# Kernel tuning notes

Hardware: AMD Instinct MI355X
Metric: run time of the kernel (lower is better)

The kernel has to match this reference:

```python
import jax, jax.numpy as jnp
from jax import lax
import numpy as np

DN = ('NCDHW', 'OIDHW', 'NCDHW')


def _conv3(x, w, b):
    # standard 3x3x3 conv, stride 1, pad 1
    y = lax.conv_general_dilated(x, w, (1, 1, 1), ((1, 1), (1, 1), (1, 1)), dimension_numbers=DN)
    return y + b[None, :, None, None, None]


def _bn(x, gamma, beta, eps=1e-5):
    # training-mode batchnorm over (N, D, H, W), biased variance (torch semantics)
    mean = jnp.mean(x, axis=(0, 2, 3, 4), keepdims=True)
    var = jnp.var(x, axis=(0, 2, 3, 4), keepdims=True)
    return gamma[None, :, None, None, None] * (x - mean) * lax.rsqrt(var + eps) + beta[None, :, None, None, None]


def _deform_conv(x, off, w):
    # ConvOffset3d: one scalar offset per deformable group shifting the temporal (D)
    # sampling position of every kernel tap; linear interpolation along D, zero padding.
    N, C, D, H, W = x.shape
    G = off.shape[1]
    cpg = C // G
    offc = jnp.repeat(off, cpg, axis=1)                        # [N,C,D,H,W]
    base = offc + jnp.arange(D, dtype=x.dtype)[None, None, :, None, None]
    out = None
    for kd in range(3):                                        # 3 temporal taps
        pos = base + (kd - 1)                                  # fractional sample pos along D
        f0 = jnp.floor(pos)
        frac = pos - f0
        i0 = f0.astype(jnp.int32)
        i1 = i0 + 1
        m0 = ((i0 >= 0) & (i0 < D)).astype(x.dtype)
        m1 = ((i1 >= 0) & (i1 < D)).astype(x.dtype)
        g = (jnp.take_along_axis(x, jnp.clip(i0, 0, D - 1), axis=2) * ((1.0 - frac) * m0)
             + jnp.take_along_axis(x, jnp.clip(i1, 0, D - 1), axis=2) * (frac * m1))
        # the D-shift for tap kd is already baked into g -> conv with kernel (1,3,3)
        y = lax.conv_general_dilated(g, w[:, :, kd:kd + 1], (1, 1, 1), ((0, 0), (1, 1), (1, 1)), dimension_numbers=DN)
        out = y if out is None else out + y
    return out


def setup_inputs() -> dict:
    key = jax.random.key(0)
    ks = jax.random.split(key, 4)
    C, cpg = 64, 8
    N, D, H, W = 8, 16, 56, 56
    G = C // cpg
    s = 1.0 / np.sqrt(C * 27).astype(np.float32)
    x = jax.random.normal(ks[0], (N, C, D, H, W), jnp.float32)
    w_off = jax.random.normal(ks[1], (G, C, 3, 3, 3), jnp.float32) * s
    b_off = jnp.zeros((G,), jnp.float32)
    w1 = jax.random.normal(ks[2], (C, C, 3, 3, 3), jnp.float32) * s
    w2 = jax.random.normal(ks[3], (C, C, 3, 3, 3), jnp.float32) * s
    b2 = jnp.zeros((C,), jnp.float32)
    return dict(x=x, w_off=w_off, b_off=b_off, w1=w1, w2=w2, b2=b2,
                bn1_gamma=jnp.ones((C,), jnp.float32), bn1_beta=jnp.zeros((C,), jnp.float32),
                bn2_gamma=jnp.ones((C,), jnp.float32), bn2_beta=jnp.zeros((C,), jnp.float32))


def reference(x, w_off, b_off, w1, w2, b2, bn1_gamma, bn1_beta, bn2_gamma, bn2_beta):
    off = _conv3(x, w_off, b_off)               # [N, G, D, H, W]
    out = _deform_conv(x, off, w1)              # deformable conv (no bias)
    out = jax.nn.relu(_bn(out, bn1_gamma, bn1_beta))
    out = _conv3(out, w2, b2)
    out = _bn(out, bn2_gamma, bn2_beta) + x     # residual
    out = jax.nn.relu(out)
    return (out, off)
```

## Files before the change

kernel.cpp:

```cpp
#include <hip/hip_runtime.h>

#define HW 3136
#define DHW 50176
#define NEL 25690112
#define CNT 401408.0f

typedef __attribute__((ext_vector_type(8))) short          short8;
typedef __attribute__((ext_vector_type(8))) unsigned short ushort8;
typedef __attribute__((ext_vector_type(4))) float          f32x4;

__device__ __forceinline__ unsigned f2bf(float f) {
    union { float f; unsigned u; } v; v.f = f;
    return (v.u + 0x7FFFu + ((v.u >> 16) & 1u)) >> 16;
}
__device__ __forceinline__ float bf2f(unsigned u) {
    union { unsigned u; float f; } v; v.u = u << 16;
    return v.f;
}
__device__ __forceinline__ unsigned cvt_pk_bf16(float lo, float hi) {
    unsigned r;
    asm("v_cvt_pk_bf16_f32 %0, %1, %2" : "=v"(r) : "v"(lo), "v"(hi));
    return r;
}

__device__ __forceinline__ void xcd_decode(int& h, int& d, int& n, int& bucket) {
    const int bid = blockIdx.x + 56 * (blockIdx.y + 16 * blockIdx.z);
    bucket = bid & 63;
    const int swz = (bid & 7) * 896 + (bid >> 3);
    h = swz % 56;
    const int dn = swz / 56;
    d = dn & 15;
    n = dn >> 4;
}

__global__ __launch_bounds__(256) void k_transpose(
    const float* __restrict__ x, unsigned short* __restrict__ xt)
{
    __shared__ unsigned lds[4][64 * 36];
    const int d = blockIdx.x, n = blockIdx.y, z = blockIdx.z;
    const int wave = threadIdx.x >> 6, lane = threadIdx.x & 63;
    const float* xb = x + (size_t)n * 64 * DHW + d * HW;
    unsigned short* xtb = xt + (size_t)n * DHW * 64;
    unsigned* L = lds[wave];

    for (int c = z * 7 + wave; c < z * 7 + 7 && c < 49; c += 4) {
        const int P = c * 64;
#pragma unroll 4
        for (int cp = 0; cp < 32; ++cp) {
            const float a = xb[(size_t)(2 * cp) * DHW + P + lane];
            const float b = xb[(size_t)(2 * cp + 1) * DHW + P + lane];
            L[lane * 36 + cp] = cvt_pk_bf16(a, b);
        }
#pragma unroll
        for (int k = 0; k < 8; ++k) {
            const int r = (lane >> 3) + 8 * k;
            const uint4 v = *(const uint4*)&L[r * 36 + 4 * (lane & 7)];
            *(uint4*)((char*)xtb + ((size_t)(P + r) * 16 + d) * 128 + (lane & 7) * 16) = v;
        }
    }
}

__global__ __launch_bounds__(256) void k_wprep(
    const float* __restrict__ w_off, const float* __restrict__ w1,
    const float* __restrict__ w2, unsigned short* __restrict__ BtO,
    unsigned short* __restrict__ Bt1, unsigned short* __restrict__ Bt2)
{
    const int i = blockIdx.x * 256 + threadIdx.x;
    if (i < 27648) {
        const int tap = i / 1024, r = i - tap * 1024;
        const int ks = r >> 9, r3 = r & 511, lane = r3 >> 3, e = r3 & 7;
        const int row = lane & 15;
        const int ci  = ks * 32 + (lane >> 4) * 8 + e;
        BtO[i] = (row < 8) ? (unsigned short)f2bf(w_off[(row * 64 + ci) * 27 + tap]) : 0;
    }
    if (i < 110592) {
        const int tap = i / 4096, r = i - tap * 4096;
        const int rg = r >> 10, r2 = r & 1023;
        const int ks = r2 >> 9, r3 = r2 & 511, lane = r3 >> 3, e = r3 & 7;
        const int co = rg * 16 + (lane & 15);
        const int ci = ks * 32 + (lane >> 4) * 8 + e;
        Bt1[i] = (unsigned short)f2bf(w1[(co * 64 + ci) * 27 + tap]);
        Bt2[i] = (unsigned short)f2bf(w2[(co * 64 + ci) * 27 + tap]);
    }
}

template<int NCO, bool BN, bool DIN>
__global__ __launch_bounds__(512) void k_conv(
    const unsigned short* __restrict__ src, const unsigned short* __restrict__ Bt,
    const float* __restrict__ bias, const float* __restrict__ scv,
    const float* __restrict__ shv, float* __restrict__ dst,
    float* __restrict__ osum, float* __restrict__ osq)
{
    __shared__ unsigned short A[538 * 72];
    int h, d, n, bucket;
    xcd_decode(h, d, n, bucket);
    const int tid = threadIdx.x;
    const int wave = tid >> 6, lane = tid & 63, lm = lane & 15, quad = lane >> 4;
    const int k8 = tid & 7;

    float scr[8], shr[8];
    if constexpr (BN) {
#pragma unroll
        for (int e = 0; e < 8; ++e) { scr[e] = scv[k8 * 8 + e]; shr[e] = shv[k8 * 8 + e]; }
    }

    const unsigned short* snb = DIN ? (src + (size_t)n * DHW * 64)
                                    : (src + (size_t)(n * 16) * HW * 64);

    const int spx = tid >> 3;
    const int wq  = spx - 1;
    const bool pxok = (tid < 464) & ((unsigned)wq < 56u);
#pragma unroll
    for (int row = 0; row < 9; ++row) {
        const int kd = row / 3, kh = row - (row / 3) * 3;
        const int dq = d + kd - 1, hq = h + kh - 1;
        uint4 pk = {0u, 0u, 0u, 0u};
        if (pxok & ((unsigned)dq < 16u) & ((unsigned)hq < 56u)) {
            const size_t off = DIN ? (((size_t)(hq * 56 + wq) * 16 + dq) * 64)
                                   : (((size_t)dq * HW + hq * 56 + wq) * 64);
            const ushort8 val = *(const ushort8*)(snb + off + k8 * 8);
            if constexpr (BN) {
                float f[8];
#pragma unroll
                for (int e = 0; e < 8; ++e)
                    f[e] = fmaxf(fmaf(bf2f(val[e]), scr[e], shr[e]), 0.f);
                pk.x = cvt_pk_bf16(f[0], f[1]);
                pk.y = cvt_pk_bf16(f[2], f[3]);
                pk.z = cvt_pk_bf16(f[4], f[5]);
                pk.w = cvt_pk_bf16(f[6], f[7]);
            } else {
                pk = *(const uint4*)&val;
            }
        }
        if (tid < 464) *(uint4*)&A[(size_t)(row * 58 + spx) * 72 + k8 * 8] = pk;
    }
    __syncthreads();

    if constexpr (NCO == 8) {
        const int ksw = wave >> 2, mf = wave & 3;
        f32x4 acc = (f32x4){0.f, 0.f, 0.f, 0.f};
        const unsigned short* Btb = Bt + ksw * 512;
        unsigned boff = (unsigned)lane * 8;
        short8 bc = *(const short8*)(Btb + boff);
        boff += 1024u;
        unsigned arow = (unsigned)(mf * 16 + lm) * 72 + quad * 8 + ksw * 32;
#pragma unroll 1
        for (int r9 = 0; r9 < 9; ++r9) {
#pragma unroll
            for (int kw = 0; kw < 3; ++kw) {
                const bool more = (kw < 2) | (r9 < 8);
                short8 bn;
                if (more) bn = *(const short8*)(Btb + boff);
                const short8 a = *(const short8*)&A[arow + kw * 72];
                acc = __builtin_amdgcn_mfma_f32_16x16x32_bf16(a, bc, acc, 0, 0, 0);
                if (more) { bc = bn; boff += 1024u; }
            }
            arow += 58 * 72;
        }
        __syncthreads();
        float* E = (float*)A;
#pragma unroll
        for (int r = 0; r < 4; ++r) {
            const int mm = mf * 16 + quad * 4 + r;
            if (mm < 56) E[ksw * 952 + mm * 17 + lm] = acc[r];
        }
        __syncthreads();
        if (lane < 56) {
            const float v = E[lane * 17 + wave] + E[952 + lane * 17 + wave] + bias[wave];
            dst[((size_t)(n * 8 + wave) * 16 + d) * HW + h * 56 + lane] = v;
        }
    } else {
        const int mf0 = (wave & 1) * 2, nf0 = wave >> 1;
        f32x4 acc[2];
        acc[0] = (f32x4){0.f, 0.f, 0.f, 0.f};
        acc[1] = (f32x4){0.f, 0.f, 0.f, 0.f};

        const unsigned short* Btb = Bt + (unsigned)nf0 * 1024;
        unsigned boff = (unsigned)lane * 8;
        short8 bc0 = *(const short8*)(Btb + boff);
        short8 bc1 = *(const short8*)(Btb + boff + 512);
        boff += 4096u;
        unsigned arow = (unsigned)(mf0 * 16 + lm) * 72 + quad * 8;

#pragma unroll 1
        for (int r9 = 0; r9 < 9; ++r9) {
#pragma unroll
            for (int kw = 0; kw < 3; ++kw) {
                const bool more = (kw < 2) | (r9 < 8);
                short8 bn0, bn1;
                if (more) {
                    bn0 = *(const short8*)(Btb + boff);
                    bn1 = *(const short8*)(Btb + boff + 512);
                }
                const unsigned ab = arow + kw * 72;
                const short8 a00 = *(const short8*)&A[ab];
                const short8 a01 = *(const short8*)&A[ab + 1152];
                const short8 a10 = *(const short8*)&A[ab + 32];
                const short8 a11 = *(const short8*)&A[ab + 1152 + 32];
                acc[0] = __builtin_amdgcn_mfma_f32_16x16x32_bf16(a00, bc0, acc[0], 0, 0, 0);
                acc[1] = __builtin_amdgcn_mfma_f32_16x16x32_bf16(a01, bc0, acc[1], 0, 0, 0);
                acc[0] = __builtin_amdgcn_mfma_f32_16x16x32_bf16(a10, bc1, acc[0], 0, 0, 0);
                acc[1] = __builtin_amdgcn_mfma_f32_16x16x32_bf16(a11, bc1, acc[1], 0, 0, 0);
                if (more) { bc0 = bn0; bc1 = bn1; boff += 4096u; }
            }
            arow += 58 * 72;
        }

        __syncthreads();
        float* E = (float*)A;
#pragma unroll
        for (int mf = 0; mf < 2; ++mf)
#pragma unroll
            for (int r = 0; r < 4; ++r) {
                const int mm = (mf0 + mf) * 16 + quad * 4 + r;
                if (mm < 56) E[mm * 65 + nf0 * 16 + lm] = acc[mf][r];
            }
        __syncthreads();
        const int co = tid >> 3, w8 = tid & 7;
        const float bco = bias[co];
        float* drow = &dst[((size_t)(n * 64 + co) * 16 + d) * HW + h * 56];
        float s = 0.f, q = 0.f;
#pragma unroll
        for (int i = 0; i < 7; ++i) {
            const int w0 = w8 + 8 * i;
            const float v = E[w0 * 65 + co] + bco;
            drow[w0] = v;
            s += v; q = fmaf(v, v, q);
        }
        s += __shfl_down(s, 1); q += __shfl_down(q, 1);
        s += __shfl_down(s, 2); q += __shfl_down(q, 2);
        s += __shfl_down(s, 4); q += __shfl_down(q, 4);
        if ((lane & 7) == 0) {
            atomicAdd(&osum[(bucket << 6) + co], s);
            atomicAdd(&osq [(bucket << 6) + co], q);
        }
    }
}

__global__ __launch_bounds__(512) void k_deform(
    const unsigned short* __restrict__ xt, const float* __restrict__ offo,
    const unsigned short* __restrict__ Bt, unsigned short* __restrict__ out1,
    float* __restrict__ osum, float* __restrict__ osq)
{
    __shared__ unsigned short A[538 * 72];
    int h, d, n, bucket;
    xcd_decode(h, d, n, bucket);
    const int tid = threadIdx.x;
    const int wave = tid >> 6, lane = tid & 63, lm = lane & 15, quad = lane >> 4;

    float pv[3];
#pragma unroll
    for (int it = 0; it < 3; ++it) {
        const int c = tid + it * 512;
        float p = 0.f;
        if (c < 1392) {
            const int g = c & 7, pix = c >> 3;
            const int hq3 = pix / 58, px = pix - hq3 * 58;
            const int habs = h + hq3 - 1, wq = px - 1;
            if (((unsigned)habs < 56u) & ((unsigned)wq < 56u))
                p = offo[((size_t)(n * 8 + g) * 16 + d) * HW + habs * 56 + wq] + (float)d;
        }
        pv[it] = p;
    }

#pragma unroll
    for (int it = 0; it < 3; ++it) {
        const int c = tid + it * 512;
        if (c >= 1392) break;
        const int g = c & 7, pix = c >> 3;
        const int hq3 = pix / 58, px = pix - hq3 * 58;
        const int habs = h + hq3 - 1, wq = px - 1;
        uint4 p0 = {0u,0u,0u,0u}, p1 = {0u,0u,0u,0u}, p2 = {0u,0u,0u,0u};
        if (((unsigned)habs < 56u) & ((unsigned)wq < 56u)) {
            const float p = pv[it];
            const float fl = floorf(p);
            const float fr = p - fl;
            const int i0 = (int)fl;
            const unsigned short* cb = xt + ((size_t)n * HW + habs * 56 + wq) * (16 * 64) + g * 8;
            float sv[4][8], m[4];
#pragma unroll
            for (int j = 0; j < 4; ++j) {
                const int dj = i0 - 1 + j;
                const bool ok = (unsigned)dj < 16u;
                m[j] = ok ? 1.f : 0.f;
                const ushort8 v = *(const ushort8*)(cb + (size_t)(ok ? dj : 0) * 64);
#pragma unroll
                for (int e = 0; e < 8; ++e) sv[j][e] = bf2f(v[e]);
            }
            const float fi = 1.f - fr;
            const float w0a = fi * m[0], w0b = fr * m[1];
            const float w1a = fi * m[1], w1b = fr * m[2];
            const float w2a = fi * m[2], w2b = fr * m[3];
            float a0[8], a1[8], a2[8];
#pragma unroll
            for (int e = 0; e < 8; ++e) {
                a0[e] = fmaf(sv[1][e], w0b, sv[0][e] * w0a);
                a1[e] = fmaf(sv[2][e], w1b, sv[1][e] * w1a);
                a2[e] = fmaf(sv[3][e], w2b, sv[2][e] * w2a);
            }
            p0.x = cvt_pk_bf16(a0[0], a0[1]); p0.y = cvt_pk_bf16(a0[2], a0[3]);
            p0.z = cvt_pk_bf16(a0[4], a0[5]); p0.w = cvt_pk_bf16(a0[6], a0[7]);
            p1.x = cvt_pk_bf16(a1[0], a1[1]); p1.y = cvt_pk_bf16(a1[2], a1[3]);
            p1.z = cvt_pk_bf16(a1[4], a1[5]); p1.w = cvt_pk_bf16(a1[6], a1[7]);
            p2.x = cvt_pk_bf16(a2[0], a2[1]); p2.y = cvt_pk_bf16(a2[2], a2[3]);
            p2.z = cvt_pk_bf16(a2[4], a2[5]); p2.w = cvt_pk_bf16(a2[6], a2[7]);
        }
        const int sl = hq3 * 58 + px;
        *(uint4*)&A[(size_t)(sl          ) * 72 + g * 8] = p0;
        *(uint4*)&A[(size_t)(sl + 3 * 58 ) * 72 + g * 8] = p1;
        *(uint4*)&A[(size_t)(sl + 6 * 58 ) * 72 + g * 8] = p2;
    }
    __syncthreads();

    const int mf0 = (wave & 1) * 2, nf0 = wave >> 1;
    f32x4 acc[2];
    acc[0] = (f32x4){0.f, 0.f, 0.f, 0.f};
    acc[1] = (f32x4){0.f, 0.f, 0.f, 0.f};

    const unsigned short* Btb = Bt + (unsigned)nf0 * 1024;
    unsigned boff = (unsigned)lane * 8;
    short8 bc0 = *(const short8*)(Btb + boff);
    short8 bc1 = *(const short8*)(Btb + boff + 512);
    boff += 4096u;
    unsigned arow = (unsigned)(mf0 * 16 + lm) * 72 + quad * 8;

#pragma unroll 1
    for (int r9 = 0; r9 < 9; ++r9) {
#pragma unroll
        for (int kw = 0; kw < 3; ++kw) {
            const bool more = (kw < 2) | (r9 < 8);
            short8 bn0, bn1;
            if (more) {
                bn0 = *(const short8*)(Btb + boff);
                bn1 = *(const short8*)(Btb + boff + 512);
            }
            const unsigned ab = arow + kw * 72;
            const short8 a00 = *(const short8*)&A[ab];
            const short8 a01 = *(const short8*)&A[ab + 1152];
            const short8 a10 = *(const short8*)&A[ab + 32];
            const short8 a11 = *(const short8*)&A[ab + 1152 + 32];
            acc[0] = __builtin_amdgcn_mfma_f32_16x16x32_bf16(a00, bc0, acc[0], 0, 0, 0);
            acc[1] = __builtin_amdgcn_mfma_f32_16x16x32_bf16(a01, bc0, acc[1], 0, 0, 0);
            acc[0] = __builtin_amdgcn_mfma_f32_16x16x32_bf16(a10, bc1, acc[0], 0, 0, 0);
            acc[1] = __builtin_amdgcn_mfma_f32_16x16x32_bf16(a11, bc1, acc[1], 0, 0, 0);
            if (more) { bc0 = bn0; bc1 = bn1; boff += 4096u; }
        }
        arow += 58 * 72;
    }

    __syncthreads();
#pragma unroll
    for (int mf = 0; mf < 2; ++mf)
#pragma unroll
        for (int r = 0; r < 4; ++r) {
            const int mm = (mf0 + mf) * 16 + quad * 4 + r;
            if (mm < 56)
                A[mm * 72 + nf0 * 16 + lm] = (unsigned short)f2bf(acc[mf][r]);
        }
    __syncthreads();
    const size_t pixb = ((size_t)(n * 16) + d) * HW + h * 56;
    if (tid < 448) {
        const int px = tid >> 3, kk = tid & 7;
        *(uint4*)(out1 + (pixb + px) * 64 + kk * 8) = *(const uint4*)&A[px * 72 + kk * 8];
    }
    const int co = tid >> 3, w8 = tid & 7;
    float s = 0.f, q = 0.f;
#pragma unroll
    for (int i = 0; i < 7; ++i) {
        const int w0 = w8 + 8 * i;
        const float v = bf2f(A[w0 * 72 + co]);
        s += v; q = fmaf(v, v, q);
    }
    s += __shfl_down(s, 1); q += __shfl_down(q, 1);
    s += __shfl_down(s, 2); q += __shfl_down(q, 2);
    s += __shfl_down(s, 4); q += __shfl_down(q, 4);
    if ((lane & 7) == 0) {
        atomicAdd(&osum[(bucket << 6) + co], s);
        atomicAdd(&osq [(bucket << 6) + co], q);
    }
}

__global__ void k_finalize(const float* __restrict__ sums, const float* __restrict__ sqs,
                           const float* __restrict__ gamma, const float* __restrict__ beta,
                           float* __restrict__ scale, float* __restrict__ shift)
{
    const int c = threadIdx.x;
    float s = 0.f, q = 0.f;
#pragma unroll 8
    for (int b = 0; b < 64; ++b) {
        s += sums[(b << 6) + c];
        q += sqs [(b << 6) + c];
    }
    const float mean = s / CNT;
    const float var  = q / CNT - mean * mean;
    const float sc   = gamma[c] * rsqrtf(var + 1e-5f);
    scale[c] = sc;
    shift[c] = fmaf(-mean, sc, beta[c]);
}

__global__ __launch_bounds__(256) void k_residual(
    float4* __restrict__ dst, const float4* __restrict__ raw,
    const float4* __restrict__ x,
    const float* __restrict__ scale, const float* __restrict__ shift)
{
    const int i = blockIdx.x * 256 + threadIdx.x;
    const int c = (i / 12544) & 63;
    const float sc = scale[c], sh = shift[c];
    float4 v = raw[i];
    const float4 xv = x[i];
    v.x = fmaxf(fmaf(v.x, sc, sh) + xv.x, 0.f);
    v.y = fmaxf(fmaf(v.y, sc, sh) + xv.y, 0.f);
    v.z = fmaxf(fmaf(v.z, sc, sh) + xv.z, 0.f);
    v.w = fmaxf(fmaf(v.w, sc, sh) + xv.w, 0.f);
    dst[i] = v;
}

extern "C" void kernel_launch(void* const* d_in, const int* in_sizes, int n_in,
                              void* d_out, int out_size, void* d_ws, size_t ws_size,
                              hipStream_t stream) {
    const float* x     = (const float*)d_in[0];
    const float* w_off = (const float*)d_in[1];
    const float* b_off = (const float*)d_in[2];
    const float* w1    = (const float*)d_in[3];
    const float* w2    = (const float*)d_in[4];
    const float* b2    = (const float*)d_in[5];
    const float* g1    = (const float*)d_in[6];
    const float* be1   = (const float*)d_in[7];
    const float* g2    = (const float*)d_in[8];
    const float* be2   = (const float*)d_in[9];

    float* out     = (float*)d_out;
    float* off_out = out + NEL;
    unsigned short* out1 = (unsigned short*)d_out;
    unsigned short* wb   = (unsigned short*)(out + 13000000);
    unsigned short* BtO  = wb;
    unsigned short* Bt1  = BtO + 27648;
    unsigned short* Bt2  = Bt1 + 110592;

    unsigned short* xt  = (unsigned short*)d_ws;
    float*          raw = (float*)d_ws;

    float* stb = (float*)((char*)d_out + 53000000);
    float* dsum = stb,        * dsq = stb + 4096;
    float* csum = stb + 8192, * csq = stb + 12288;
    float* shp = (float*)d_ws + NEL;
    float* sc1 = shp,       * sh1 = shp + 64;
    float* sc2 = shp + 128, * sh2 = shp + 192;

    hipMemsetAsync(stb, 0, 16384 * sizeof(float), stream);

    k_transpose<<<dim3(16, 8, 7), 256, 0, stream>>>(x, xt);
    k_wprep<<<432, 256, 0, stream>>>(w_off, w1, w2, BtO, Bt1, Bt2);

    const dim3 cgrid(56, 16, 8);
    k_conv<8, false, true><<<cgrid, 512, 0, stream>>>(xt, BtO, b_off, nullptr, nullptr, off_out, nullptr, nullptr);
    k_deform<<<cgrid, 512, 0, stream>>>(xt, off_out, Bt1, out1, dsum, dsq);

    k_finalize<<<1, 64, 0, stream>>>(dsum, dsq, g1, be1, sc1, sh1);

    k_conv<64, true, false><<<cgrid, 512, 0, stream>>>(out1, Bt2, b2, sc1, sh1, raw, csum, csq);

    k_finalize<<<1, 64, 0, stream>>>(csum, csq, g2, be2, sc2, sh2);
    k_residual<<<25088, 256, 0, stream>>>((float4*)out, (const float4*)raw, (const float4*)x, sc2, sh2);
}
```

Before: 656.8 us.

## Use 32x32x16 MFMA with split-K across waves in conv and deform GEMMs

Replaces the 16x16x32 bf16 MFMA tiling (each wave owning a 32px x 16co tile) with 32x32x16 MFMA tiles. Each wave now owns 32 pixels x 32 output channels over half of the input channels, and the two K halves are summed through shared memory in the epilogue. The weight prep layout is rearranged to match. This halves A-operand LDS reads per MFMA and uses the larger instruction's higher operand reuse, at the cost of an extra fp32 LDS reduction. The deform epilogue also changes from storing bf16 to fp32 partials before statistics, which slightly alters the rounding of the BN statistics.

New measurement: 663.2 us, median of 2. No clear change (+1.0%).

```diff
diff --git a/kernel.cpp b/kernel.cpp
--- a/kernel.cpp
+++ b/kernel.cpp
@@ -5,9 +5,10 @@
 #define NEL 25690112
 #define CNT 401408.0f
 
-typedef __attribute__((ext_vector_type(8))) short          short8;
-typedef __attribute__((ext_vector_type(8))) unsigned short ushort8;
-typedef __attribute__((ext_vector_type(4))) float          f32x4;
+typedef __attribute__((ext_vector_type(8)))  short          short8;
+typedef __attribute__((ext_vector_type(8)))  unsigned short ushort8;
+typedef __attribute__((ext_vector_type(4)))  float          f32x4;
+typedef __attribute__((ext_vector_type(16))) float          f32x16;
 
 __device__ __forceinline__ unsigned f2bf(float f) {
     union { float f; unsigned u; } v; v.f = f;
@@ -75,10 +76,12 @@
     }
     if (i < 110592) {
         const int tap = i / 4096, r = i - tap * 4096;
-        const int rg = r >> 10, r2 = r & 1023;
-        const int ks = r2 >> 9, r3 = r2 & 511, lane = r3 >> 3, e = r3 & 7;
-        const int co = rg * 16 + (lane & 15);
-        const int ci = ks * 32 + (lane >> 4) * 8 + e;
+        const int cog = r >> 11, r2 = r & 2047;
+        const int ksw = r2 >> 10, r3 = r2 & 1023;
+        const int ksub = r3 >> 9, r4 = r3 & 511;
+        const int lane = r4 >> 3, e = r4 & 7;
+        const int co = cog * 32 + (lane & 31);
+        const int ci = ksw * 32 + ksub * 16 + (lane >> 5) * 8 + e;
         Bt1[i] = (unsigned short)f2bf(w1[(co * 64 + ci) * 27 + tap]);
         Bt2[i] = (unsigned short)f2bf(w2[(co * 64 + ci) * 27 + tap]);
     }
@@ -170,17 +173,16 @@
             dst[((size_t)(n * 8 + wave) * 16 + d) * HW + h * 56 + lane] = v;
         }
     } else {
-        const int mf0 = (wave & 1) * 2, nf0 = wave >> 1;
-        f32x4 acc[2];
-        acc[0] = (f32x4){0.f, 0.f, 0.f, 0.f};
-        acc[1] = (f32x4){0.f, 0.f, 0.f, 0.f};
-
-        const unsigned short* Btb = Bt + (unsigned)nf0 * 1024;
+        const int pxg = wave & 1, cog = (wave >> 1) & 1, ksw = wave >> 2;
+        f32x16 acc = (f32x16){0.f,0.f,0.f,0.f,0.f,0.f,0.f,0.f,
+                              0.f,0.f,0.f,0.f,0.f,0.f,0.f,0.f};
+
+        const unsigned short* Btb = Bt + (unsigned)(cog * 2 + ksw) * 1024;
         unsigned boff = (unsigned)lane * 8;
         short8 bc0 = *(const short8*)(Btb + boff);
         short8 bc1 = *(const short8*)(Btb + boff + 512);
         boff += 4096u;
-        unsigned arow = (unsigned)(mf0 * 16 + lm) * 72 + quad * 8;
+        unsigned arow = (unsigned)(pxg * 32 + (lane & 31)) * 72 + ksw * 32 + (lane >> 5) * 8;
 
 #pragma unroll 1
         for (int r9 = 0; r9 < 9; ++r9) {
@@ -193,14 +195,10 @@
                     bn1 = *(const short8*)(Btb + boff + 512);
                 }
                 const unsigned ab = arow + kw * 72;
-                const short8 a00 = *(const short8*)&A[ab];
-                const short8 a01 = *(const short8*)&A[ab + 1152];
-                const short8 a10 = *(const short8*)&A[ab + 32];
-                const short8 a11 = *(const short8*)&A[ab + 1152 + 32];
-                acc[0] = __builtin_amdgcn_mfma_f32_16x16x32_bf16(a00, bc0, acc[0], 0, 0, 0);
-                acc[1] = __builtin_amdgcn_mfma_f32_16x16x32_bf16(a01, bc0, acc[1], 0, 0, 0);
-                acc[0] = __builtin_amdgcn_mfma_f32_16x16x32_bf16(a10, bc1, acc[0], 0, 0, 0);
-                acc[1] = __builtin_amdgcn_mfma_f32_16x16x32_bf16(a11, bc1, acc[1], 0, 0, 0);
+                const short8 a0 = *(const short8*)&A[ab];
+                const short8 a1 = *(const short8*)&A[ab + 16];
+                acc = __builtin_amdgcn_mfma_f32_32x32x16_bf16(a0, bc0, acc, 0, 0, 0);
+                acc = __builtin_amdgcn_mfma_f32_32x32x16_bf16(a1, bc1, acc, 0, 0, 0);
                 if (more) { bc0 = bn0; bc1 = bn1; boff += 4096u; }
             }
             arow += 58 * 72;
@@ -209,12 +207,10 @@
         __syncthreads();
         float* E = (float*)A;
 #pragma unroll
-        for (int mf = 0; mf < 2; ++mf)
-#pragma unroll
-            for (int r = 0; r < 4; ++r) {
-                const int mm = (mf0 + mf) * 16 + quad * 4 + r;
-                if (mm < 56) E[mm * 65 + nf0 * 16 + lm] = acc[mf][r];
-            }
+        for (int reg = 0; reg < 16; ++reg) {
+            const int pl = (reg & 3) + 8 * (reg >> 2) + 4 * (lane >> 5);
+            E[ksw * 4160 + (pxg * 32 + pl) * 65 + cog * 32 + (lane & 31)] = acc[reg];
+        }
         __syncthreads();
         const int co = tid >> 3, w8 = tid & 7;
         const float bco = bias[co];
@@ -223,7 +219,7 @@
 #pragma unroll
         for (int i = 0; i < 7; ++i) {
             const int w0 = w8 + 8 * i;
-            const float v = E[w0 * 65 + co] + bco;
+            const float v = E[w0 * 65 + co] + E[4160 + w0 * 65 + co] + bco;
             drow[w0] = v;
             s += v; q = fmaf(v, v, q);
         }
@@ -246,7 +242,7 @@
     int h, d, n, bucket;
     xcd_decode(h, d, n, bucket);
     const int tid = threadIdx.x;
-    const int wave = tid >> 6, lane = tid & 63, lm = lane & 15, quad = lane >> 4;
+    const int wave = tid >> 6, lane = tid & 63;
 
     float pv[3];
 #pragma unroll
@@ -312,17 +308,16 @@
     }
     __syncthreads();
 
-    const int mf0 = (wave & 1) * 2, nf0 = wave >> 1;
-    f32x4 acc[2];
-    acc[0] = (f32x4){0.f, 0.f, 0.f, 0.f};
-    acc[1] = (f32x4){0.f, 0.f, 0.f, 0.f};
-
-    const unsigned short* Btb = Bt + (unsigned)nf0 * 1024;
+    const int pxg = wave & 1, cog = (wave >> 1) & 1, ksw = wave >> 2;
+    f32x16 acc = (f32x16){0.f,0.f,0.f,0.f,0.f,0.f,0.f,0.f,
+                          0.f,0.f,0.f,0.f,0.f,0.f,0.f,0.f};
+
+    const unsigned short* Btb = Bt + (unsigned)(cog * 2 + ksw) * 1024;
     unsigned boff = (unsigned)lane * 8;
     short8 bc0 = *(const short8*)(Btb + boff);
     short8 bc1 = *(const short8*)(Btb + boff + 512);
     boff += 4096u;
-    unsigned arow = (unsigned)(mf0 * 16 + lm) * 72 + quad * 8;
+    unsigned arow = (unsigned)(pxg * 32 + (lane & 31)) * 72 + ksw * 32 + (lane >> 5) * 8;
 
 #pragma unroll 1
     for (int r9 = 0; r9 < 9; ++r9) {
@@ -335,40 +330,41 @@
                 bn1 = *(const short8*)(Btb + boff + 512);
             }
             const unsigned ab = arow + kw * 72;
-            const short8 a00 = *(const short8*)&A[ab];
-            const short8 a01 = *(const short8*)&A[ab + 1152];
-            const short8 a10 = *(const short8*)&A[ab + 32];
-            const short8 a11 = *(const short8*)&A[ab + 1152 + 32];
-            acc[0] = __builtin_amdgcn_mfma_f32_16x16x32_bf16(a00, bc0, acc[0], 0, 0, 0);
-            acc[1] = __builtin_amdgcn_mfma_f32_16x16x32_bf16(a01, bc0, acc[1], 0, 0, 0);
-            acc[0] = __builtin_amdgcn_mfma_f32_16x16x32_bf16(a10, bc1, acc[0], 0, 0, 0);
-            acc[1] = __builtin_amdgcn_mfma_f32_16x16x32_bf16(a11, bc1, acc[1], 0, 0, 0);
+            const short8 a0 = *(const short8*)&A[ab];
+            const short8 a1 = *(const short8*)&A[ab + 16];
+            acc = __builtin_amdgcn_mfma_f32_32x32x16_bf16(a0, bc0, acc, 0, 0, 0);
+            acc = __builtin_amdgcn_mfma_f32_32x32x16_bf16(a1, bc1, acc, 0, 0, 0);
             if (more) { bc0 = bn0; bc1 = bn1; boff += 4096u; }
         }
         arow += 58 * 72;
     }
 
     __syncthreads();
-#pragma unroll
-    for (int mf = 0; mf < 2; ++mf)
-#pragma unroll
-        for (int r = 0; r < 4; ++r) {
-            const int mm = (mf0 + mf) * 16 + quad * 4 + r;
-            if (mm < 56)
-                A[mm * 72 + nf0 * 16 + lm] = (unsigned short)f2bf(acc[mf][r]);
-        }
+    float* E = (float*)A;
+#pragma unroll
+    for (int reg = 0; reg < 16; ++reg) {
+        const int pl = (reg & 3) + 8 * (reg >> 2) + 4 * (lane >> 5);
+        E[ksw * 4160 + (pxg * 32 + pl) * 65 + cog * 32 + (lane & 31)] = acc[reg];
+    }
     __syncthreads();
     const size_t pixb = ((size_t)(n * 16) + d) * HW + h * 56;
     if (tid < 448) {
         const int px = tid >> 3, kk = tid & 7;
-        *(uint4*)(out1 + (pixb + px) * 64 + kk * 8) = *(const uint4*)&A[px * 72 + kk * 8];
+        float v[8];
+#pragma unroll
+        for (int e = 0; e < 8; ++e)
+            v[e] = E[px * 65 + kk * 8 + e] + E[4160 + px * 65 + kk * 8 + e];
+        uint4 pk;
+        pk.x = cvt_pk_bf16(v[0], v[1]); pk.y = cvt_pk_bf16(v[2], v[3]);
+        pk.z = cvt_pk_bf16(v[4], v[5]); pk.w = cvt_pk_bf16(v[6], v[7]);
+        *(uint4*)(out1 + (pixb + px) * 64 + kk * 8) = pk;
     }
     const int co = tid >> 3, w8 = tid & 7;
     float s = 0.f, q = 0.f;
 #pragma unroll
     for (int i = 0; i < 7; ++i) {
         const int w0 = w8 + 8 * i;
-        const float v = bf2f(A[w0 * 72 + co]);
+        const float v = E[w0 * 65 + co] + E[4160 + w0 * 65 + co];
         s += v; q = fmaf(v, v, q);
     }
     s += __shfl_down(s, 1); q += __shfl_down(q, 1);
```
